# Kernel tuning notes

Measured on AMD Instinct MI355X. Metric: run time of the kernel, lower is better.

## Reference

```python
import jax, jax.numpy as jnp
import numpy as np

TAU = 0.02
M = 5  # len(modality_types) + 1; modality 0 == padding


def setup_inputs() -> dict:
    B, Q, S, D = 64, 32, 256, 128
    key = jax.random.key(0)
    k0, k1, k2, k3, k4 = jax.random.split(key, 5)
    q = jax.random.normal(k0, (B, Q, D), dtype=jnp.float32)
    q = q / jnp.linalg.norm(q, axis=-1, keepdims=True)
    d = jax.random.normal(k1, (B, S, D), dtype=jnp.float32)
    d = d / jnp.linalg.norm(d, axis=-1, keepdims=True)
    # guarantee every modality 0..M-1 appears in each doc (first M tokens)
    head = jnp.tile(jnp.arange(M, dtype=jnp.int32), (B, 1))
    rest = jax.random.randint(k2, (B, S - M), 0, M, dtype=jnp.int32)
    modality_ids = jnp.concatenate([head, rest], axis=1)
    query_types = jax.random.randint(k3, (B,), 1, M, dtype=jnp.int32)  # in [1, M-1]
    lengths = jax.random.randint(k4, (B,), Q // 2, Q + 1)
    query_mask = jnp.arange(Q)[None, :] < lengths[:, None]
    return {"query_emb": q, "doc_emb": d, "modality_ids": modality_ids,
            "query_types": query_types, "query_mask": query_mask}


def _loss(query_emb, doc_emb, modality_ids, query_types, query_mask):
    B = query_emb.shape[0]
    idx = jnp.arange(B)
    # token-level similarity: (B, C, Q, S)
    base = jnp.einsum('bqd,csd->bcqs', query_emb, doc_emb)
    qnorm = jnp.maximum(query_mask.sum(axis=1), 1).astype(base.dtype)  # (B,)

    # agg (ColBERT max-sim): max over non-pad doc tokens, masked query sum
    nonpad = (modality_ids != 0)[None, :, None, :]
    agg_max = jnp.where(nonpad, base, -jnp.inf).max(axis=-1)           # (B, C, Q)
    sim = (agg_max * query_mask[:, None, :].astype(base.dtype)).sum(axis=-1)
    sim = sim / qnorm[:, None]                                          # (B, C)

    # _all_modality_sims: segmented max over s per modality, then sum over q
    per_mod = []
    for m in range(M):
        mask_m = (modality_ids == m)[None, :, None, :]
        per_mod.append(jnp.where(mask_m, base, -jnp.inf).max(axis=-1).sum(axis=-1))
    sims = jnp.stack(per_mod, axis=-1)                                  # (B, C, M)
    sims = sims / qnorm[:, None, None]

    # replace diagonal with the query's own modality score
    sim_fixed = sim.at[idx, idx].set(sims[idx, idx, query_types])

    # hard negatives: all (doc, modality) pairs except pad modality and own positive
    all_modal = sims.reshape(B, B * M)
    keep_mask = jnp.ones((B, B * M), dtype=bool)
    keep_mask = keep_mask.at[:, 0::M].set(False)
    keep_mask = keep_mask.at[idx, idx * M + query_types].set(False)
    n_keep = B * M - B - 1  # exact per-row count (query_types >= 1, no overlap)
    order = jnp.argsort((~keep_mask).astype(jnp.int32), axis=1, stable=True)[:, :n_keep]
    extras = jnp.take_along_axis(all_modal, order, axis=1)              # (B, n_keep)

    logits = jnp.concatenate([sim_fixed, extras], axis=1) / TAU
    # cross entropy with labels = arange(B) (positive is column b)
    return (jax.nn.logsumexp(logits, axis=1) - logits[idx, idx]).mean()


def reference(query_emb, doc_emb, modality_ids, query_types, query_mask):
    return _loss(query_emb, doc_emb, modality_ids, query_types, query_mask)
```

## Files before the change

kernel.cpp:

```cpp
#include <hip/hip_runtime.h>
#include <math.h>

#define TAU_F 0.02f
#define NB 64
#define NQ 32
#define NS 256
#define ND 128
#define MAXT 12
#define PERMSTRIDE 384

typedef __bf16 bf16x8 __attribute__((ext_vector_type(8)));
typedef float f32x16 __attribute__((ext_vector_type(16)));

#define OFF_TILEMOD 0u
#define OFF_TCOUNT  4096u
#define OFF_DFRAG   16384u
#define OFF_QFRAG   6307840u
#define OFF_SIMOUT  6832128u

__global__ __launch_bounds__(256) void
prep_frag_kernel(const float* __restrict__ qemb, const float* __restrict__ demb,
                 const int* __restrict__ mod,
                 __bf16* __restrict__ qfrag, __bf16* __restrict__ dfrag,
                 int* __restrict__ tilemod_g, int* __restrict__ tcount_g) {
    int blk = blockIdx.x;
    int tid = threadIdx.x;
    int lane = tid & 63, wv = tid >> 6;
    int li32 = lane & 31, kh = lane >> 5;

    if (blk >= NB) {
        int b = blk - NB;
#pragma unroll
        for (int i = 0; i < 2; ++i) {
            int kc = wv * 2 + i;
            int k0 = kc * 16 + kh * 8;
            const float* src = qemb + ((size_t)b * NQ + li32) * ND + k0;
            float4 a = *(const float4*)src;
            float4 bq = *(const float4*)(src + 4);
            bf16x8 o;
            o[0] = (__bf16)a.x;  o[1] = (__bf16)a.y;  o[2] = (__bf16)a.z;  o[3] = (__bf16)a.w;
            o[4] = (__bf16)bq.x; o[5] = (__bf16)bq.y; o[6] = (__bf16)bq.z; o[7] = (__bf16)bq.w;
            *(bf16x8*)(qfrag + (((size_t)b * 8 + kc) * 64 + lane) * 8) = o;
        }
        return;
    }

    int c = blk;
    __shared__ int smod[NS];
    __shared__ int sperm[PERMSTRIDE];
    __shared__ int counts[5], firsts[5], offs[5], padded[5];
    __shared__ int stilemod[MAXT];
    __shared__ int sT;

    if (tid < 5) { counts[tid] = 0; firsts[tid] = NS; }
    __syncthreads();
    int m_tok = mod[c * NS + tid];
    smod[tid] = m_tok;
    if (m_tok) { atomicAdd(&counts[m_tok], 1); atomicMin(&firsts[m_tok], tid); }
    __syncthreads();
    if (tid == 0) {
        int pos = 0;
        for (int m = 1; m <= 4; ++m) {
            offs[m] = pos;
            int p = (counts[m] + 31) & ~31;
            padded[m] = p;
            for (int t = pos >> 5; t < (pos + p) >> 5; ++t) stilemod[t] = m;
            pos += p;
        }
        sT = pos >> 5;
        tcount_g[c] = pos >> 5;
    }
    __syncthreads();
    if (m_tok) {
        int rank = 0;
        for (int s = 0; s < tid; ++s) rank += (smod[s] == m_tok);
        sperm[offs[m_tok] + rank] = tid;
    }
    if (tid < 4) {
        int m = tid + 1;
        for (int p = counts[m]; p < padded[m]; ++p) sperm[offs[m] + p] = firsts[m];
    }
    __syncthreads();
    int T = sT;
    if (tid < T) tilemod_g[c * MAXT + tid] = stilemod[tid];

    for (int kc = wv; kc < 8; kc += 4) {
        int k0 = kc * 16 + kh * 8;
        for (int t = 0; t < T; ++t) {
            int srow = sperm[t * 32 + li32];
            const float* src = demb + ((size_t)c * NS + srow) * ND + k0;
            float4 a = *(const float4*)src;
            float4 bq = *(const float4*)(src + 4);
            bf16x8 o;
            o[0] = (__bf16)a.x;  o[1] = (__bf16)a.y;  o[2] = (__bf16)a.z;  o[3] = (__bf16)a.w;
            o[4] = (__bf16)bq.x; o[5] = (__bf16)bq.y; o[6] = (__bf16)bq.z; o[7] = (__bf16)bq.w;
            *(bf16x8*)(dfrag + (((size_t)(c * MAXT + t) * 8 + kc) * 64 + lane) * 8) = o;
        }
    }
}

__global__ __launch_bounds__(256) void
main_kernel(const __bf16* __restrict__ dfrag, const __bf16* __restrict__ qfrag,
            const int* __restrict__ tilemod, const int* __restrict__ tcount,
            const int* __restrict__ qmask, float* __restrict__ simout) {
    int blk = blockIdx.x;
    int c  = (blk & 7) * 8 + (blk >> 8);
    int bp = (blk >> 3) & 31;
    int b0 = bp * 2;
    int tid = threadIdx.x;
    int lane = tid & 63, wv = tid >> 6;

    bf16x8 bfrag[2][8];
#pragma unroll
    for (int bi = 0; bi < 2; ++bi)
#pragma unroll
        for (int kc = 0; kc < 8; ++kc)
            bfrag[bi][kc] = *(const bf16x8*)(qfrag + (((size_t)(b0 + bi) * 8 + kc) * 64 + lane) * 8);

    float vmax[2][4];
#pragma unroll
    for (int bi = 0; bi < 2; ++bi)
#pragma unroll
        for (int m = 0; m < 4; ++m) vmax[bi][m] = -1e30f;

    int T = tcount[c];
    for (int t = wv; t < T; t += 4) {
        bf16x8 af[8];
#pragma unroll
        for (int kc = 0; kc < 8; ++kc)
            af[kc] = *(const bf16x8*)(dfrag + (((size_t)(c * MAXT + t) * 8 + kc) * 64 + lane) * 8);
        int tm = tilemod[c * MAXT + t];
#pragma unroll
        for (int bi = 0; bi < 2; ++bi) {
            f32x16 acc = {0.f,0.f,0.f,0.f,0.f,0.f,0.f,0.f,0.f,0.f,0.f,0.f,0.f,0.f,0.f,0.f};
#pragma unroll
            for (int kc = 0; kc < 8; ++kc)
                acc = __builtin_amdgcn_mfma_f32_32x32x16_bf16(af[kc], bfrag[bi][kc], acc, 0, 0, 0);
            float v = acc[0];
#pragma unroll
            for (int r = 1; r < 16; ++r) v = fmaxf(v, acc[r]);
            v = fmaxf(v, __shfl_xor(v, 32, 64));
            switch (tm) {
            case 1:  vmax[bi][0] = fmaxf(vmax[bi][0], v); break;
            case 2:  vmax[bi][1] = fmaxf(vmax[bi][1], v); break;
            case 3:  vmax[bi][2] = fmaxf(vmax[bi][2], v); break;
            default: vmax[bi][3] = fmaxf(vmax[bi][3], v); break;
            }
        }
    }

    __shared__ float lv[4][2][4][32];
    if (lane < 32) {
#pragma unroll
        for (int bi = 0; bi < 2; ++bi)
#pragma unroll
            for (int m = 0; m < 4; ++m) lv[wv][bi][m][lane] = vmax[bi][m];
    }
    __syncthreads();
    __shared__ float l2[2][4][32];
    {
        int bi = tid >> 7, m = (tid >> 5) & 3, q = tid & 31;
        float v = fmaxf(fmaxf(lv[0][bi][m][q], lv[1][bi][m][q]),
                        fmaxf(lv[2][bi][m][q], lv[3][bi][m][q]));
        l2[bi][m][q] = v;
    }
    __syncthreads();
    if (tid < 64) {
        int bi = tid >> 5, q = tid & 31;
        float m1 = l2[bi][0][q], m2 = l2[bi][1][q];
        float m3 = l2[bi][2][q], m4 = l2[bi][3][q];
        int b = b0 + bi;
        float agg = fmaxf(fmaxf(m1, m2), fmaxf(m3, m4));
        float s0 = (qmask[b * NQ + q] != 0) ? agg : 0.f;
        float s1 = m1, s2 = m2, s3 = m3, s4 = m4;
#pragma unroll
        for (int off = 16; off >= 1; off >>= 1) {
            s0 += __shfl_xor(s0, off, 64);
            s1 += __shfl_xor(s1, off, 64);
            s2 += __shfl_xor(s2, off, 64);
            s3 += __shfl_xor(s3, off, 64);
            s4 += __shfl_xor(s4, off, 64);
        }
        if (q == 0) {
            float* o = simout + ((size_t)b * NB + c) * 5;
            o[0] = s0; o[1] = s1; o[2] = s2; o[3] = s3; o[4] = s4;
        }
    }
}

__global__ void loss_kernel(const float* __restrict__ simout, const int* __restrict__ qtypes,
                            const int* __restrict__ qmask, float* __restrict__ out) {
    __shared__ float lloss[NB];
    int tid = threadIdx.x;
    int r = tid >> 2, i = tid & 3;
    int cnt = 0;
#pragma unroll
    for (int j = 0; j < 8; ++j) cnt += (qmask[r * NQ + i * 8 + j] != 0);
    cnt += __shfl_xor(cnt, 1, 64);
    cnt += __shfl_xor(cnt, 2, 64);
    float scale = 1.0f / (TAU_F * (float)(cnt > 0 ? cnt : 1));

    float mx = -1e30f;
    for (int cc = 0; cc < 16; ++cc) {
        int c = i * 16 + cc;
        const float* p = simout + ((size_t)r * NB + c) * 5;
#pragma unroll
        for (int j = 0; j < 5; ++j) {
            if (j == 0 && c == r) continue;
            mx = fmaxf(mx, p[j] * scale);
        }
    }
    mx = fmaxf(mx, __shfl_xor(mx, 1, 64));
    mx = fmaxf(mx, __shfl_xor(mx, 2, 64));
    float sum = 0.f;
    for (int cc = 0; cc < 16; ++cc) {
        int c = i * 16 + cc;
        const float* p = simout + ((size_t)r * NB + c) * 5;
#pragma unroll
        for (int j = 0; j < 5; ++j) {
            if (j == 0 && c == r) continue;
            sum += expf(p[j] * scale - mx);
        }
    }
    sum += __shfl_xor(sum, 1, 64);
    sum += __shfl_xor(sum, 2, 64);
    if (i == 0) {
        float pos = simout[((size_t)r * NB + r) * 5 + qtypes[r]] * scale;
        lloss[r] = logf(sum) + mx - pos;
    }
    __syncthreads();
    if (tid == 0) {
        float s = 0.f;
        for (int r2 = 0; r2 < NB; ++r2) s += lloss[r2];
        out[0] = s * (1.0f / NB);
    }
}

extern "C" void kernel_launch(void* const* d_in, const int* in_sizes, int n_in,
                              void* d_out, int out_size, void* d_ws, size_t ws_size,
                              hipStream_t stream) {
    const float* qemb   = (const float*)d_in[0];
    const float* demb   = (const float*)d_in[1];
    const int*   mod    = (const int*)d_in[2];
    const int*   qtypes = (const int*)d_in[3];
    const int*   qmask  = (const int*)d_in[4];

    char* ws = (char*)d_ws;
    int*    tilemod = (int*)(ws + OFF_TILEMOD);
    int*    tcount  = (int*)(ws + OFF_TCOUNT);
    __bf16* dfrag   = (__bf16*)(ws + OFF_DFRAG);
    __bf16* qfrag   = (__bf16*)(ws + OFF_QFRAG);
    float*  simout  = (float*)(ws + OFF_SIMOUT);

    prep_frag_kernel<<<2 * NB, 256, 0, stream>>>(qemb, demb, mod, qfrag, dfrag,
                                                 tilemod, tcount);
    main_kernel<<<2048, 256, 0, stream>>>(dfrag, qfrag, tilemod, tcount, qmask, simout);
    loss_kernel<<<1, 256, 0, stream>>>(simout, qtypes, qmask, (float*)d_out);
}
```

Baseline: 101.8 us.

## Fuse prep into main kernel with on-the-fly bf16 conversion and ballot-based permutation

Removes the separate prep kernel and its global workspace round-trip. Each main-kernel block now reads fp32 query and doc rows directly and converts them to bf16 fragments in registers. It also builds the per-modality token permutation in shared memory, using wave ballots and popcounts in place of a serial rank loop. This saves one launch and the write and reread of the fragment buffers. In exchange, every one of the 2048 blocks redoes the permutation and the conversion, and reads twice as many bytes per doc row through gathered, less coalesced loads.

```diff
diff --git a/kernel.cpp b/kernel.cpp
--- a/kernel.cpp
+++ b/kernel.cpp
@@ -12,124 +12,113 @@
 typedef __bf16 bf16x8 __attribute__((ext_vector_type(8)));
 typedef float f32x16 __attribute__((ext_vector_type(16)));
 
-#define OFF_TILEMOD 0u
-#define OFF_TCOUNT  4096u
-#define OFF_DFRAG   16384u
-#define OFF_QFRAG   6307840u
-#define OFF_SIMOUT  6832128u
+#define OFF_SIMOUT  0u
 
 __global__ __launch_bounds__(256) void
-prep_frag_kernel(const float* __restrict__ qemb, const float* __restrict__ demb,
-                 const int* __restrict__ mod,
-                 __bf16* __restrict__ qfrag, __bf16* __restrict__ dfrag,
-                 int* __restrict__ tilemod_g, int* __restrict__ tcount_g) {
-    int blk = blockIdx.x;
-    int tid = threadIdx.x;
-    int lane = tid & 63, wv = tid >> 6;
-    int li32 = lane & 31, kh = lane >> 5;
-
-    if (blk >= NB) {
-        int b = blk - NB;
-#pragma unroll
-        for (int i = 0; i < 2; ++i) {
-            int kc = wv * 2 + i;
-            int k0 = kc * 16 + kh * 8;
-            const float* src = qemb + ((size_t)b * NQ + li32) * ND + k0;
-            float4 a = *(const float4*)src;
-            float4 bq = *(const float4*)(src + 4);
-            bf16x8 o;
-            o[0] = (__bf16)a.x;  o[1] = (__bf16)a.y;  o[2] = (__bf16)a.z;  o[3] = (__bf16)a.w;
-            o[4] = (__bf16)bq.x; o[5] = (__bf16)bq.y; o[6] = (__bf16)bq.z; o[7] = (__bf16)bq.w;
-            *(bf16x8*)(qfrag + (((size_t)b * 8 + kc) * 64 + lane) * 8) = o;
-        }
-        return;
-    }
-
-    int c = blk;
-    __shared__ int smod[NS];
-    __shared__ int sperm[PERMSTRIDE];
-    __shared__ int counts[5], firsts[5], offs[5], padded[5];
-    __shared__ int stilemod[MAXT];
-    __shared__ int sT;
-
-    if (tid < 5) { counts[tid] = 0; firsts[tid] = NS; }
-    __syncthreads();
-    int m_tok = mod[c * NS + tid];
-    smod[tid] = m_tok;
-    if (m_tok) { atomicAdd(&counts[m_tok], 1); atomicMin(&firsts[m_tok], tid); }
-    __syncthreads();
-    if (tid == 0) {
-        int pos = 0;
-        for (int m = 1; m <= 4; ++m) {
-            offs[m] = pos;
-            int p = (counts[m] + 31) & ~31;
-            padded[m] = p;
-            for (int t = pos >> 5; t < (pos + p) >> 5; ++t) stilemod[t] = m;
-            pos += p;
-        }
-        sT = pos >> 5;
-        tcount_g[c] = pos >> 5;
-    }
-    __syncthreads();
-    if (m_tok) {
-        int rank = 0;
-        for (int s = 0; s < tid; ++s) rank += (smod[s] == m_tok);
-        sperm[offs[m_tok] + rank] = tid;
-    }
-    if (tid < 4) {
-        int m = tid + 1;
-        for (int p = counts[m]; p < padded[m]; ++p) sperm[offs[m] + p] = firsts[m];
-    }
-    __syncthreads();
-    int T = sT;
-    if (tid < T) tilemod_g[c * MAXT + tid] = stilemod[tid];
-
-    for (int kc = wv; kc < 8; kc += 4) {
-        int k0 = kc * 16 + kh * 8;
-        for (int t = 0; t < T; ++t) {
-            int srow = sperm[t * 32 + li32];
-            const float* src = demb + ((size_t)c * NS + srow) * ND + k0;
-            float4 a = *(const float4*)src;
-            float4 bq = *(const float4*)(src + 4);
-            bf16x8 o;
-            o[0] = (__bf16)a.x;  o[1] = (__bf16)a.y;  o[2] = (__bf16)a.z;  o[3] = (__bf16)a.w;
-            o[4] = (__bf16)bq.x; o[5] = (__bf16)bq.y; o[6] = (__bf16)bq.z; o[7] = (__bf16)bq.w;
-            *(bf16x8*)(dfrag + (((size_t)(c * MAXT + t) * 8 + kc) * 64 + lane) * 8) = o;
-        }
-    }
-}
-
-__global__ __launch_bounds__(256) void
-main_kernel(const __bf16* __restrict__ dfrag, const __bf16* __restrict__ qfrag,
-            const int* __restrict__ tilemod, const int* __restrict__ tcount,
-            const int* __restrict__ qmask, float* __restrict__ simout) {
+fused_kernel(const float* __restrict__ qemb, const float* __restrict__ demb,
+             const int* __restrict__ mod, const int* __restrict__ qmask,
+             float* __restrict__ simout) {
     int blk = blockIdx.x;
     int c  = (blk & 7) * 8 + (blk >> 8);
     int bp = (blk >> 3) & 31;
     int b0 = bp * 2;
     int tid = threadIdx.x;
     int lane = tid & 63, wv = tid >> 6;
+    int li32 = lane & 31, kh = lane >> 5;
 
     bf16x8 bfrag[2][8];
 #pragma unroll
+    for (int bi = 0; bi < 2; ++bi) {
+        const float* qb = qemb + ((size_t)(b0 + bi) * NQ + li32) * ND + kh * 8;
+#pragma unroll
+        for (int kc = 0; kc < 8; ++kc) {
+            float4 a = *(const float4*)(qb + kc * 16);
+            float4 b2 = *(const float4*)(qb + kc * 16 + 4);
+            bf16x8 o;
+            o[0] = (__bf16)a.x;  o[1] = (__bf16)a.y;  o[2] = (__bf16)a.z;  o[3] = (__bf16)a.w;
+            o[4] = (__bf16)b2.x; o[5] = (__bf16)b2.y; o[6] = (__bf16)b2.z; o[7] = (__bf16)b2.w;
+            bfrag[bi][kc] = o;
+        }
+    }
+
+    __shared__ int sperm[PERMSTRIDE];
+    __shared__ int stilemod[MAXT];
+    __shared__ int wcnt[4][4];
+    __shared__ int firsts[4];
+    __shared__ int sT;
+
+    if (tid < 4) firsts[tid] = NS;
+    __syncthreads();
+    int m_tok = mod[c * NS + tid];
+    unsigned long long mk1 = __ballot(m_tok == 1);
+    unsigned long long mk2 = __ballot(m_tok == 2);
+    unsigned long long mk3 = __ballot(m_tok == 3);
+    unsigned long long mk4 = __ballot(m_tok == 4);
+    if (lane == 0) {
+        wcnt[wv][0] = __popcll(mk1); wcnt[wv][1] = __popcll(mk2);
+        wcnt[wv][2] = __popcll(mk3); wcnt[wv][3] = __popcll(mk4);
+    }
+    if (m_tok) atomicMin(&firsts[m_tok - 1], tid);
+    __syncthreads();
+
+    int cnt1 = wcnt[0][0] + wcnt[1][0] + wcnt[2][0] + wcnt[3][0];
+    int cnt2 = wcnt[0][1] + wcnt[1][1] + wcnt[2][1] + wcnt[3][1];
+    int cnt3 = wcnt[0][2] + wcnt[1][2] + wcnt[2][2] + wcnt[3][2];
+    int cnt4 = wcnt[0][3] + wcnt[1][3] + wcnt[2][3] + wcnt[3][3];
+    int pad1 = (cnt1 + 31) & ~31, pad2 = (cnt2 + 31) & ~31;
+    int pad3 = (cnt3 + 31) & ~31, pad4 = (cnt4 + 31) & ~31;
+    int off1 = 0, off2 = pad1, off3 = pad2 + off2, off4 = pad3 + off3;
+    int total = off4 + pad4;
+    if (tid == 0) sT = total >> 5;
+
+    if (m_tok) {
+        unsigned long long mk = (m_tok == 1) ? mk1 : (m_tok == 2) ? mk2
+                              : (m_tok == 3) ? mk3 : mk4;
+        int off = (m_tok == 1) ? off1 : (m_tok == 2) ? off2
+                : (m_tok == 3) ? off3 : off4;
+        int rank = __popcll(mk & ((1ull << lane) - 1ull));
+        for (int w = 0; w < 4; ++w)
+            if (w < wv) rank += wcnt[w][m_tok - 1];
+        sperm[off + rank] = tid;
+    }
+    if (tid < 128) {
+        int m = tid >> 5, p = tid & 31;
+        int cm = (m == 0) ? cnt1 : (m == 1) ? cnt2 : (m == 2) ? cnt3 : cnt4;
+        int pm = (m == 0) ? pad1 : (m == 1) ? pad2 : (m == 2) ? pad3 : pad4;
+        int om = (m == 0) ? off1 : (m == 1) ? off2 : (m == 2) ? off3 : off4;
+        int slot = cm + p;
+        if (slot < pm) sperm[om + slot] = firsts[m];
+    }
+    if (tid < MAXT) {
+        int t0 = tid * 32;
+        int m = 4;
+        if (t0 < off2) m = 1; else if (t0 < off3) m = 2; else if (t0 < off4) m = 3;
+        stilemod[tid] = m;
+    }
+    __syncthreads();
+
+    float vmax[2][4];
+#pragma unroll
     for (int bi = 0; bi < 2; ++bi)
 #pragma unroll
-        for (int kc = 0; kc < 8; ++kc)
-            bfrag[bi][kc] = *(const bf16x8*)(qfrag + (((size_t)(b0 + bi) * 8 + kc) * 64 + lane) * 8);
-
-    float vmax[2][4];
-#pragma unroll
-    for (int bi = 0; bi < 2; ++bi)
-#pragma unroll
         for (int m = 0; m < 4; ++m) vmax[bi][m] = -1e30f;
 
-    int T = tcount[c];
+    int T = sT;
+    const float* dbase = demb + (size_t)c * NS * ND + kh * 8;
     for (int t = wv; t < T; t += 4) {
+        int r32 = sperm[t * 32 + li32];
+        const float* rowp = dbase + (size_t)r32 * ND;
         bf16x8 af[8];
 #pragma unroll
-        for (int kc = 0; kc < 8; ++kc)
-            af[kc] = *(const bf16x8*)(dfrag + (((size_t)(c * MAXT + t) * 8 + kc) * 64 + lane) * 8);
-        int tm = tilemod[c * MAXT + t];
+        for (int kc = 0; kc < 8; ++kc) {
+            float4 a = *(const float4*)(rowp + kc * 16);
+            float4 b2 = *(const float4*)(rowp + kc * 16 + 4);
+            bf16x8 o;
+            o[0] = (__bf16)a.x;  o[1] = (__bf16)a.y;  o[2] = (__bf16)a.z;  o[3] = (__bf16)a.w;
+            o[4] = (__bf16)b2.x; o[5] = (__bf16)b2.y; o[6] = (__bf16)b2.z; o[7] = (__bf16)b2.w;
+            af[kc] = o;
+        }
+        int tm = stilemod[t];
 #pragma unroll
         for (int bi = 0; bi < 2; ++bi) {
             f32x16 acc = {0.f,0.f,0.f,0.f,0.f,0.f,0.f,0.f,0.f,0.f,0.f,0.f,0.f,0.f,0.f,0.f};
@@ -157,18 +146,18 @@
             for (int m = 0; m < 4; ++m) lv[wv][bi][m][lane] = vmax[bi][m];
     }
     __syncthreads();
-    __shared__ float l2[2][4][32];
+    __shared__ float l2s[2][4][32];
     {
         int bi = tid >> 7, m = (tid >> 5) & 3, q = tid & 31;
         float v = fmaxf(fmaxf(lv[0][bi][m][q], lv[1][bi][m][q]),
                         fmaxf(lv[2][bi][m][q], lv[3][bi][m][q]));
-        l2[bi][m][q] = v;
+        l2s[bi][m][q] = v;
     }
     __syncthreads();
     if (tid < 64) {
         int bi = tid >> 5, q = tid & 31;
-        float m1 = l2[bi][0][q], m2 = l2[bi][1][q];
-        float m3 = l2[bi][2][q], m4 = l2[bi][3][q];
+        float m1 = l2s[bi][0][q], m2 = l2s[bi][1][q];
+        float m3 = l2s[bi][2][q], m4 = l2s[bi][3][q];
         int b = b0 + bi;
         float agg = fmaxf(fmaxf(m1, m2), fmaxf(m3, m4));
         float s0 = (qmask[b * NQ + q] != 0) ? agg : 0.f;
@@ -246,14 +235,8 @@
     const int*   qmask  = (const int*)d_in[4];
 
     char* ws = (char*)d_ws;
-    int*    tilemod = (int*)(ws + OFF_TILEMOD);
-    int*    tcount  = (int*)(ws + OFF_TCOUNT);
-    __bf16* dfrag   = (__bf16*)(ws + OFF_DFRAG);
-    __bf16* qfrag   = (__bf16*)(ws + OFF_QFRAG);
-    float*  simout  = (float*)(ws + OFF_SIMOUT);
-
-    prep_frag_kernel<<<2 * NB, 256, 0, stream>>>(qemb, demb, mod, qfrag, dfrag,
-                                                 tilemod, tcount);
-    main_kernel<<<2048, 256, 0, stream>>>(dfrag, qfrag, tilemod, tcount, qmask, simout);
+    float* simout = (float*)(ws + OFF_SIMOUT);
+
+    fused_kernel<<<2048, 256, 0, stream>>>(qemb, demb, mod, qmask, simout);
     loss_kernel<<<1, 256, 0, stream>>>(simout, qtypes, qmask, (float*)d_out);
 }
```

Measured after the change: 139.9 us. 1.37x slower.
